# Optimization experiments

Hardware: AMD Instinct MI355X
Metric: run time of the kernel (lower is better)

## Reference

```python
import jax, jax.numpy as jnp
import numpy as np

QUALITY = 8
N_PART = 18000 * QUALITY ** 2  # 1,152,000
N_GRID = 128 * QUALITY         # 1024
DX = 1.0 / N_GRID
INV_DX = float(N_GRID)
DT = 1e-4 / QUALITY
P_VOL = (DX * 0.5) ** 2
P_MASS = P_VOL * 1.0
E_MOD, NU = 5000.0, 0.2
MU0 = E_MOD / (2.0 * (1.0 + NU))
LAM0 = E_MOD * NU / ((1.0 + NU) * (1.0 - 2.0 * NU))
OFF = jnp.array([[i, j] for i in range(3) for j in range(3)], dtype=jnp.int32)  # [9,2]


def setup_inputs() -> dict:
    key = jax.random.key(0)
    ks = jax.random.split(key, 6)
    x = 0.05 + 0.9 * jax.random.uniform(ks[0], (N_PART, 2), dtype=jnp.float32)
    v = jax.random.normal(ks[1], (N_PART, 2), dtype=jnp.float32)
    C = 0.1 * jax.random.normal(ks[2], (N_PART, 2, 2), dtype=jnp.float32)
    F = jnp.eye(2, dtype=jnp.float32) + 0.02 * jax.random.normal(ks[3], (N_PART, 2, 2), dtype=jnp.float32)
    material = jax.random.randint(ks[4], (N_PART,), 0, 3, dtype=jnp.int32)
    Jp = 0.5 + jax.random.uniform(ks[5], (N_PART,), dtype=jnp.float32)
    gravity = jnp.array([0.0, -1.0], dtype=jnp.float32)
    attractor_strength = jnp.array(1.0, dtype=jnp.float32)
    attractor_pos = jnp.array([0.5, 0.5], dtype=jnp.float32)
    return dict(x=x, v=v, C=C, F=F, Jp=Jp, gravity=gravity,
                attractor_strength=attractor_strength, attractor_pos=attractor_pos,
                material=material)


def _substep(x, v, C, F, Jp, gravity, attractor_strength, attractor_pos, material):
    I2 = jnp.eye(2, dtype=x.dtype)
    # ---- per-particle quadratic B-spline weights ----
    base = jnp.floor(x * INV_DX - 0.5).astype(jnp.int32)            # [P,2]
    fx = x * INV_DX - base.astype(x.dtype)                           # [P,2]
    w = jnp.stack([0.5 * (1.5 - fx) ** 2,
                   0.75 - (fx - 1.0) ** 2,
                   0.5 * (fx - 0.5) ** 2], axis=1)                   # [P,3,2]
    weight = w[:, OFF[:, 0], 0] * w[:, OFF[:, 1], 1]                 # [P,9]

    # ---- deformation update + elastoplastic stress ----
    F = jnp.einsum('pij,pjk->pik', I2 + DT * C, F)                   # [P,2,2]
    h = jnp.clip(jnp.exp(10.0 * (1.0 - Jp)), 0.1, 5.0)
    h = jnp.where(material == 1, 0.3, h)
    mu = jnp.where(material == 0, 0.0, MU0 * h)                      # [P]
    la = LAM0 * h
    U, sig, Vh = jnp.linalg.svd(F)                                   # sig [P,2]
    new_sig = jnp.where((material == 2)[:, None],
                        jnp.clip(sig, 1.0 - 2.5e-2, 1.0 + 4.5e-3), sig)
    Jp = Jp * jnp.prod(sig / new_sig, axis=1)
    J = jnp.prod(new_sig, axis=1)                                    # [P]
    F_fluid = jnp.sqrt(J)[:, None, None] * I2
    F_snow = jnp.einsum('pij,pj,pjk->pik', U, new_sig, Vh)
    F = jnp.where((material == 0)[:, None, None], F_fluid,
                  jnp.where((material == 2)[:, None, None], F_snow, F))
    R = jnp.einsum('pij,pjk->pik', U, Vh)                            # rotation U V^T
    stress = (2.0 * mu[:, None, None] *
              jnp.einsum('pij,pkj->pik', F - R, F) +
              (la * J * (J - 1.0))[:, None, None] * I2)
    stress = (-DT * P_VOL * 4.0 * INV_DX * INV_DX) * stress
    affine = stress + P_MASS * C                                     # [P,2,2]

    # ---- P2G scatter-add ----
    dpos = (OFF.astype(x.dtype)[None] - fx[:, None, :]) * DX         # [P,9,2]
    mom = weight[:, :, None] * (P_MASS * v[:, None, :] +
                                jnp.einsum('pab,pkb->pka', affine, dpos))
    gi = jnp.clip(base[:, None, 0] + OFF[None, :, 0], 0, N_GRID - 1)
    gj = jnp.clip(base[:, None, 1] + OFF[None, :, 1], 0, N_GRID - 1)
    idx = (gi * N_GRID + gj).reshape(-1)                              # [P*9]
    grid_v = jnp.zeros((N_GRID * N_GRID, 2), x.dtype).at[idx].add(mom.reshape(-1, 2))
    grid_m = jnp.zeros((N_GRID * N_GRID,), x.dtype).at[idx].add((weight * P_MASS).reshape(-1))

    # ---- grid update ----
    gv = grid_v.reshape(N_GRID, N_GRID, 2)
    gm = grid_m.reshape(N_GRID, N_GRID)
    mask = gm > 0
    gv = jnp.where(mask[..., None], gv / jnp.where(mask, gm, 1.0)[..., None], 0.0)
    gv = gv + DT * 30.0 * gravity                                    # broadcast [2]
    ii, jj = jnp.meshgrid(jnp.arange(N_GRID), jnp.arange(N_GRID), indexing='ij')
    coords = DX * jnp.stack([ii, jj], axis=-1).astype(x.dtype)        # [G,G,2]
    dist = attractor_pos - coords
    gv = gv + dist / (0.01 + jnp.linalg.norm(dist, axis=-1, keepdims=True)) \
              * attractor_strength * DT * 100.0
    gvx, gvy = gv[..., 0], gv[..., 1]
    gvx = jnp.where((ii < 3) & (gvx < 0), 0.0, gvx)
    gvx = jnp.where((ii > N_GRID - 3) & (gvx > 0), 0.0, gvx)
    gvy = jnp.where((jj < 3) & (gvy < 0), 0.0, gvy)
    gvy = jnp.where((jj > N_GRID - 3) & (gvy > 0), 0.0, gvy)
    gv = jnp.where(mask[..., None], jnp.stack([gvx, gvy], axis=-1), 0.0)

    # ---- G2P gather ----
    g_v = gv.reshape(N_GRID * N_GRID, 2)[idx].reshape(-1, 9, 2)       # [P,9,2]
    new_v = jnp.einsum('pk,pka->pa', weight, g_v)
    dpos_g = OFF.astype(x.dtype)[None] - fx[:, None, :]               # unscaled
    new_C = 4.0 * INV_DX * jnp.einsum('pk,pka,pkb->pab', weight, g_v, dpos_g)
    x_new = x + DT * new_v
    return x_new, new_v, new_C, F, Jp


def reference(x, v, C, F, Jp, gravity, attractor_strength, attractor_pos, material):
    return _substep(x, v, C, F, Jp, gravity, attractor_strength, attractor_pos, material)
```

## Files before the change

### kernel.cpp

```cpp
#include <hip/hip_runtime.h>
#include <hip/hip_fp16.h>
#include <math.h>

namespace {
constexpr int   QUALITY = 8;
constexpr int   NPART   = 18000 * QUALITY * QUALITY;
constexpr int   NG      = 128 * QUALITY;
constexpr int   NCELL   = NG * NG;
constexpr int   CT      = 16;
constexpr int   NBT     = NG / CT;
constexpr float DX      = 1.0f / (float)NG;
constexpr float INV_DX  = (float)NG;
constexpr float DT      = (float)(1e-4 / (double)QUALITY);
constexpr float MU0     = (float)(5000.0 / (2.0 * (1.0 + 0.2)));
constexpr float LAM0    = (float)(5000.0 * 0.2 / ((1.0 + 0.2) * (1.0 - 0.4)));
constexpr float STRESS_RP  = (float)(-(1e-4 / 8.0) * 4.0 * 1024.0 * 1024.0);
constexpr float GRAV_SCALE = (float)((1e-4 / 8.0) * 30.0);
constexpr float ATTR_SCALE = (float)((1e-4 / 8.0) * 100.0);

typedef int v4i __attribute__((ext_vector_type(4)));

__device__ __forceinline__ int2 base_of(float xx, float xy) {
    int bx = (int)floorf(xx * INV_DX - 0.5f);
    int by = (int)floorf(xy * INV_DX - 0.5f);
    bx = min(max(bx, 0), NG - 3);
    by = min(max(by, 0), NG - 3);
    return make_int2(bx, by);
}

__device__ __forceinline__ unsigned pack2h(float a, float b) {
    __half2 h = __floats2half2_rn(a, b);
    return *reinterpret_cast<unsigned*>(&h);
}
__device__ __forceinline__ float2 unpack2h(unsigned u) {
    __half2 h = *reinterpret_cast<__half2*>(&u);
    return __half22float2(h);
}

__device__ __forceinline__ float bspline(float s) {
    s = fabsf(s);
    float a = 0.75f - s * s;
    float b = 1.5f - s;
    b = 0.5f * b * b;
    return (s < 0.5f) ? a : b;
}
}

__global__ __launch_bounds__(256)
void count_kernel(const float* __restrict__ x, int* __restrict__ cnt,
                  int* __restrict__ rank) {
    int p = blockIdx.x * blockDim.x + threadIdx.x;
    if (p >= NPART) return;
    const float2 xv = ((const float2*)x)[p];
    int2 b = base_of(xv.x, xv.y);
    rank[p] = atomicAdd(&cnt[b.x * NG + b.y], 1);
}

__global__ __launch_bounds__(256)
void blocksum_kernel(const int* __restrict__ cnt, int* __restrict__ bsum) {
    __shared__ int sh[256];
    int t = threadIdx.x;
    int4 c = ((const int4*)cnt)[blockIdx.x * 256 + t];
    sh[t] = c.x + c.y + c.z + c.w;
    __syncthreads();
    for (int s = 128; s > 0; s >>= 1) {
        if (t < s) sh[t] += sh[t + s];
        __syncthreads();
    }
    if (t == 0) bsum[blockIdx.x] = sh[0];
}

__global__ __launch_bounds__(1024)
void scanb_kernel(const int* __restrict__ bsum, int* __restrict__ boff,
                  int* __restrict__ cell_start) {
    __shared__ int s[1024];
    int t = threadIdx.x;
    int v = bsum[t];
    s[t] = v;
    __syncthreads();
    for (int off = 1; off < 1024; off <<= 1) {
        int add = (t >= off) ? s[t - off] : 0;
        __syncthreads();
        s[t] += add;
        __syncthreads();
    }
    boff[t] = s[t] - v;
    if (t == 1023) cell_start[NCELL] = s[t];
}

__global__ __launch_bounds__(256)
void scanc_kernel(const int* __restrict__ cnt, const int* __restrict__ boff,
                  int* __restrict__ cell_start) {
    __shared__ int tsum[256];
    int t = threadIdx.x;
    int gbase4 = blockIdx.x * 256 + t;
    int4 c = ((const int4*)cnt)[gbase4];
    int s1 = c.x, s2 = s1 + c.y, s3 = s2 + c.z, tot = s3 + c.w;
    tsum[t] = tot;
    __syncthreads();
    for (int off = 1; off < 256; off <<= 1) {
        int add = (t >= off) ? tsum[t - off] : 0;
        __syncthreads();
        tsum[t] += add;
        __syncthreads();
    }
    int excl = tsum[t] - tot;
    int g = boff[blockIdx.x] + excl;
    ((int4*)cell_start)[gbase4] = make_int4(g, g + s1, g + s2, g + s3);
}

__global__ __launch_bounds__(256)
void physics_scatter_kernel(const float* __restrict__ x, const float* __restrict__ v,
                            const float* __restrict__ Cin, const float* __restrict__ Fin,
                            const float* __restrict__ Jpin, const int* __restrict__ mat,
                            const int* __restrict__ cell_start, const int* __restrict__ rank,
                            uint4* __restrict__ spay,
                            float* __restrict__ outF, float* __restrict__ outJp)
{
    int p = blockIdx.x * blockDim.x + threadIdx.x;
    if (p >= NPART) return;

    const float2 xv = ((const float2*)x)[p];
    const float2 vv = ((const float2*)v)[p];
    const float4 Cv = ((const float4*)Cin)[p];
    const float4 Fv = ((const float4*)Fin)[p];
    float xx = xv.x, xy = xv.y;
    float C00 = Cv.x, C01 = Cv.y, C10 = Cv.z, C11 = Cv.w;
    float F00 = Fv.x, F01 = Fv.y, F10 = Fv.z, F11 = Fv.w;

    float A00 = 1.0f + DT * C00, A01 = DT * C01, A10 = DT * C10, A11 = 1.0f + DT * C11;
    float G00 = A00 * F00 + A01 * F10;
    float G01 = A00 * F01 + A01 * F11;
    float G10 = A10 * F00 + A11 * F10;
    float G11 = A10 * F01 + A11 * F11;

    int m = mat[p];
    float Jp = Jpin[p];
    float h = fminf(fmaxf(expf(10.0f * (1.0f - Jp)), 0.1f), 5.0f);
    if (m == 1) h = 0.3f;
    float mu = (m == 0) ? 0.0f : MU0 * h;
    float la = LAM0 * h;

    float Ee = 0.5f * (G00 + G11);
    float Hh = 0.5f * (G10 - G01);
    float Ff = 0.5f * (G00 - G11);
    float Gg = 0.5f * (G10 + G01);
    float Qq = sqrtf(Ee * Ee + Hh * Hh);
    float Rr = sqrtf(Ff * Ff + Gg * Gg);
    float s0 = Qq + Rr, s1 = Qq - Rr;
    float b1 = atan2f(Gg, Ff);
    float b2 = atan2f(Hh, Ee);
    float phi = 0.5f * (b1 + b2), th = 0.5f * (b1 - b2);
    float sphi, cphi, sth, cth;
    sincosf(phi, &sphi, &cphi);
    sincosf(th, &sth, &cth);

    float ns0 = s0, ns1 = s1;
    if (m == 2) {
        ns0 = fminf(fmaxf(s0, 1.0f - 2.5e-2f), 1.0f + 4.5e-3f);
        ns1 = fminf(fmaxf(s1, 1.0f - 2.5e-2f), 1.0f + 4.5e-3f);
        Jp = Jp * (s0 / ns0) * (s1 / ns1);
    }
    float J = ns0 * ns1;

    float FF00, FF01, FF10, FF11;
    if (m == 0) {
        float sj = sqrtf(J);
        FF00 = sj; FF01 = 0.0f; FF10 = 0.0f; FF11 = sj;
    } else if (m == 2) {
        FF00 = ns0 * cphi * cth + ns1 * sphi * sth;
        FF01 = ns0 * cphi * sth - ns1 * sphi * cth;
        FF10 = ns0 * sphi * cth - ns1 * cphi * sth;
        FF11 = ns0 * sphi * sth + ns1 * cphi * cth;
    } else {
        FF00 = G00; FF01 = G01; FF10 = G10; FF11 = G11;
    }

    float cr = cphi * cth + sphi * sth;
    float sr = sphi * cth - cphi * sth;

    float D00 = FF00 - cr,  D01 = FF01 + sr;
    float D10 = FF10 - sr,  D11 = FF11 - cr;
    float S00 = D00 * FF00 + D01 * FF01;
    float S01 = D00 * FF10 + D01 * FF11;
    float S10 = D10 * FF00 + D11 * FF01;
    float S11 = D10 * FF10 + D11 * FF11;
    float lj = la * J * (J - 1.0f);
    S00 = 2.0f * mu * S00 + lj;
    S01 = 2.0f * mu * S01;
    S10 = 2.0f * mu * S10;
    S11 = 2.0f * mu * S11 + lj;
    float a00 = STRESS_RP * S00 + C00;
    float a01 = STRESS_RP * S01 + C01;
    float a10 = STRESS_RP * S10 + C10;
    float a11 = STRESS_RP * S11 + C11;

    ((float4*)outF)[p] = make_float4(FF00, FF01, FF10, FF11);
    outJp[p] = Jp;

    float bxf = floorf(xx * INV_DX - 0.5f);
    float byf = floorf(xy * INV_DX - 0.5f);
    float fxx = xx * INV_DX - bxf;
    float fxy = xy * INV_DX - byf;
    unsigned qx = (unsigned)__float2int_rn((fxx - 0.5f) * 16383.0f);
    unsigned qy = (unsigned)__float2int_rn((fxy - 0.5f) * 16383.0f);

    int2 b = base_of(xx, xy);

    v4i payload;
    payload.x = (int)((qx & 0x3FFFu) | ((qy & 0x3FFFu) << 16) | (((unsigned)b.y & 3u) << 30));
    payload.y = (int)pack2h(vv.x, vv.y);
    payload.z = (int)pack2h(a00, a01);
    payload.w = (int)pack2h(a10, a11);

    int pos = cell_start[b.x * NG + b.y] + rank[p];
    __builtin_nontemporal_store(payload, (v4i*)&spay[pos]);
}

__global__ __launch_bounds__(256)
void p2g_gather_grid_kernel(const uint4* __restrict__ spay,
                            const int* __restrict__ cell_start,
                            const float* __restrict__ grav,
                            const float* __restrict__ astr,
                            const float* __restrict__ apos,
                            float* __restrict__ gv)
{
    int b = blockIdx.x;
    int tile = (b & 7) * 512 + (b >> 3);
    int lr = threadIdx.x / CT;
    int lc = threadIdx.x % CT;
    int cx = (tile / NBT) * CT + lr;
    int cy = (tile % NBT) * CT + lc;

    float svx = 0.0f, svy = 0.0f, sw = 0.0f;
    int c0 = max(cy - 2, 0);
    float fcy = (float)cy;

    #pragma unroll
    for (int d = 0; d < 3; ++d) {
        int r = cx - 2 + d;
        if (r < 0 || r > NG - 1) continue;
        int row = r * NG;
        int s = cell_start[row + c0];
        int e = cell_start[row + cy + 1];
        const float io = (float)(2 - d);
        for (int t = s; t < e; ++t) {
            uint4 q = spay[t];
            float fxx = 0.5f + (float)(q.x & 0x3FFFu) * (1.0f / 16383.0f);
            float fxy = 0.5f + (float)((q.x >> 16) & 0x3FFFu) * (1.0f / 16383.0f);
            float fj = (float)((cy - (int)(q.x >> 30)) & 3);
            float wx;
            if (d == 0)      wx = 0.5f * (fxx - 0.5f) * (fxx - 0.5f);
            else if (d == 1) wx = 0.75f - (fxx - 1.0f) * (fxx - 1.0f);
            else             wx = 0.5f * (1.5f - fxx) * (1.5f - fxx);
            float wy = bspline(fxy - fj);
            float w = wx * wy;
            float2 vv = unpack2h(q.y);
            float2 aA = unpack2h(q.z);
            float2 aB = unpack2h(q.w);
            float dpx = (io - fxx) * DX;
            float dpy = (fj - fxy) * DX;
            svx += w * (vv.x + aA.x * dpx + aA.y * dpy);
            svy += w * (vv.y + aB.x * dpx + aB.y * dpy);
            sw  += w;
        }
    }

    float vx = 0.0f, vy = 0.0f;
    if (sw > 0.0f) {
        float inv = 1.0f / sw;
        vx = svx * inv + GRAV_SCALE * grav[0];
        vy = svy * inv + GRAV_SCALE * grav[1];
        float dxp = apos[0] - DX * (float)cx;
        float dyp = apos[1] - DX * fcy;
        float nrm = sqrtf(dxp * dxp + dyp * dyp);
        float k = astr[0] * ATTR_SCALE / (0.01f + nrm);
        vx += dxp * k;
        vy += dyp * k;
        if (cx < 3 && vx < 0.0f) vx = 0.0f;
        if (cx > NG - 3 && vx > 0.0f) vx = 0.0f;
        if (cy < 3 && vy < 0.0f) vy = 0.0f;
        if (cy > NG - 3 && vy > 0.0f) vy = 0.0f;
    }
    ((float2*)gv)[cx * NG + cy] = make_float2(vx, vy);
}

__global__ __launch_bounds__(256)
void g2p_kernel(const float* __restrict__ x, const float* __restrict__ gv,
                float* __restrict__ outX, float* __restrict__ outV,
                float* __restrict__ outC)
{
    int p = blockIdx.x * blockDim.x + threadIdx.x;
    if (p >= NPART) return;

    const float2 xv = ((const float2*)x)[p];
    float xx = xv.x, xy = xv.y;
    float bxf = floorf(xx * INV_DX - 0.5f);
    float byf = floorf(xy * INV_DX - 0.5f);
    int bx = (int)bxf, by = (int)byf;
    float fxx = xx * INV_DX - bxf;
    float fxy = xy * INV_DX - byf;

    float wxs[3], wys[3];
    wxs[0] = 0.5f * (1.5f - fxx) * (1.5f - fxx);
    wxs[1] = 0.75f - (fxx - 1.0f) * (fxx - 1.0f);
    wxs[2] = 0.5f * (fxx - 0.5f) * (fxx - 0.5f);
    wys[0] = 0.5f * (1.5f - fxy) * (1.5f - fxy);
    wys[1] = 0.75f - (fxy - 1.0f) * (fxy - 1.0f);
    wys[2] = 0.5f * (fxy - 0.5f) * (fxy - 0.5f);

    int a0 = min(max(by & ~1, 0), NG - 4);
    bool odd = (by - a0) == 1;

    float nvx = 0.0f, nvy = 0.0f;
    float c00 = 0.0f, c01 = 0.0f, c10 = 0.0f, c11 = 0.0f;

    #pragma unroll
    for (int i = 0; i < 3; ++i) {
        int gi = min(max(bx + i, 0), NG - 1);
        float dpx = (float)i - fxx;
        const float4* rowp = (const float4*)(gv + gi * NG * 2 + a0 * 2);
        float4 A = rowp[0];
        float4 B = rowp[1];
        float g0x = odd ? A.z : A.x,  g0y = odd ? A.w : A.y;
        float g1x = odd ? B.x : A.z,  g1y = odd ? B.y : A.w;
        float g2x = odd ? B.z : B.x,  g2y = odd ? B.w : B.y;
        float w0 = wxs[i] * wys[0];
        float w1 = wxs[i] * wys[1];
        float w2 = wxs[i] * wys[2];
        float dpy0 = 0.0f - fxy, dpy1 = 1.0f - fxy, dpy2 = 2.0f - fxy;
        nvx += w0 * g0x + w1 * g1x + w2 * g2x;
        nvy += w0 * g0y + w1 * g1y + w2 * g2y;
        c00 += dpx * (w0 * g0x + w1 * g1x + w2 * g2x);
        c01 += w0 * g0x * dpy0 + w1 * g1x * dpy1 + w2 * g2x * dpy2;
        c10 += dpx * (w0 * g0y + w1 * g1y + w2 * g2y);
        c11 += w0 * g0y * dpy0 + w1 * g1y * dpy1 + w2 * g2y * dpy2;
    }
    float cs = 4.0f * INV_DX;
    ((float2*)outV)[p] = make_float2(nvx, nvy);
    ((float2*)outX)[p] = make_float2(xx + DT * nvx, xy + DT * nvy);
    ((float4*)outC)[p] = make_float4(cs * c00, cs * c01, cs * c10, cs * c11);
}

extern "C" void kernel_launch(void* const* d_in, const int* in_sizes, int n_in,
                              void* d_out, int out_size, void* d_ws, size_t ws_size,
                              hipStream_t stream)
{
    const float* x    = (const float*)d_in[0];
    const float* v    = (const float*)d_in[1];
    const float* C    = (const float*)d_in[2];
    const float* F    = (const float*)d_in[3];
    const float* Jp   = (const float*)d_in[4];
    const float* grav = (const float*)d_in[5];
    const float* astr = (const float*)d_in[6];
    const float* apos = (const float*)d_in[7];
    const int*   mat  = (const int*)d_in[8];

    float* out   = (float*)d_out;
    float* outX  = out;
    float* outV  = out + 2 * NPART;
    float* outC  = out + 4 * NPART;
    float* outF  = out + 8 * NPART;
    float* outJp = out + 12 * NPART;

    int*   ws_i      = (int*)d_ws;
    int*   cnt       = ws_i;
    float* gv        = (float*)d_ws;
    int*   cell_start= ws_i + 2 * NCELL;
    int*   bsum      = cell_start + NCELL + 1;
    int*   boff      = bsum + 1024;
    int*   rank      = boff + 1024;
    size_t off       = (size_t)(3 * NCELL + 2 * 1024 + 1 + NPART);
    off = (off + 3) & ~(size_t)3;
    uint4* spay      = (uint4*)(ws_i + off);

    const int TB = 256;
    hipMemsetAsync(cnt, 0, (size_t)NCELL * sizeof(int), stream);
    count_kernel   <<<(NPART + TB - 1) / TB, TB, 0, stream>>>(x, cnt, rank);
    blocksum_kernel<<<NCELL / 1024, TB, 0, stream>>>(cnt, bsum);
    scanb_kernel   <<<1, 1024, 0, stream>>>(bsum, boff, cell_start);
    scanc_kernel   <<<NCELL / 1024, TB, 0, stream>>>(cnt, boff, cell_start);
    physics_scatter_kernel<<<(NPART + TB - 1) / TB, TB, 0, stream>>>(
        x, v, C, F, Jp, mat, cell_start, rank, spay, outF, outJp);
    p2g_gather_grid_kernel<<<NBT * NBT, TB, 0, stream>>>(
        spay, cell_start, grav, astr, apos, gv);
    g2p_kernel     <<<(NPART + TB - 1) / TB, TB, 0, stream>>>(x, gv, outX, outV, outC);
}
```

Measured before the change: 181.3 us.

## Replace three-pass global scan with single-pass per-row scan and atomic row offsets

The three-kernel prefix sum (block sums, scan of block sums, final scan) is replaced by one kernel that scans each grid row locally and claims a row base offset with an atomicAdd on a global counter. Rows are no longer contiguous in global order, so cell_start becomes a per-row array with one extra end entry per row, and the scatter and gather kernels index it by row. This removes two kernel launches and their serialization, including a single-block scan. In exchange, row order in the sorted buffer is no longer deterministic and scalar stores replace the vectorized int4 stores.

```diff
diff --git a/kernel.cpp b/kernel.cpp
--- a/kernel.cpp
+++ b/kernel.cpp
@@ -7,6 +7,7 @@
 constexpr int   NPART   = 18000 * QUALITY * QUALITY;
 constexpr int   NG      = 128 * QUALITY;
 constexpr int   NCELL   = NG * NG;
+constexpr int   CSROW   = NG + 1;
 constexpr int   CT      = 16;
 constexpr int   NBT     = NG / CT;
 constexpr float DX      = 1.0f / (float)NG;
@@ -57,44 +58,13 @@
 }
 
 __global__ __launch_bounds__(256)
-void blocksum_kernel(const int* __restrict__ cnt, int* __restrict__ bsum) {
-    __shared__ int sh[256];
+void row_scan_kernel(const int* __restrict__ cnt, int* __restrict__ counter,
+                     int* __restrict__ cell_start) {
+    __shared__ int tsum[256];
+    __shared__ int s_base;
+    int r = blockIdx.x;
     int t = threadIdx.x;
-    int4 c = ((const int4*)cnt)[blockIdx.x * 256 + t];
-    sh[t] = c.x + c.y + c.z + c.w;
-    __syncthreads();
-    for (int s = 128; s > 0; s >>= 1) {
-        if (t < s) sh[t] += sh[t + s];
-        __syncthreads();
-    }
-    if (t == 0) bsum[blockIdx.x] = sh[0];
-}
-
-__global__ __launch_bounds__(1024)
-void scanb_kernel(const int* __restrict__ bsum, int* __restrict__ boff,
-                  int* __restrict__ cell_start) {
-    __shared__ int s[1024];
-    int t = threadIdx.x;
-    int v = bsum[t];
-    s[t] = v;
-    __syncthreads();
-    for (int off = 1; off < 1024; off <<= 1) {
-        int add = (t >= off) ? s[t - off] : 0;
-        __syncthreads();
-        s[t] += add;
-        __syncthreads();
-    }
-    boff[t] = s[t] - v;
-    if (t == 1023) cell_start[NCELL] = s[t];
-}
-
-__global__ __launch_bounds__(256)
-void scanc_kernel(const int* __restrict__ cnt, const int* __restrict__ boff,
-                  int* __restrict__ cell_start) {
-    __shared__ int tsum[256];
-    int t = threadIdx.x;
-    int gbase4 = blockIdx.x * 256 + t;
-    int4 c = ((const int4*)cnt)[gbase4];
+    int4 c = ((const int4*)cnt)[r * 256 + t];
     int s1 = c.x, s2 = s1 + c.y, s3 = s2 + c.z, tot = s3 + c.w;
     tsum[t] = tot;
     __syncthreads();
@@ -104,9 +74,16 @@
         tsum[t] += add;
         __syncthreads();
     }
-    int excl = tsum[t] - tot;
-    int g = boff[blockIdx.x] + excl;
-    ((int4*)cell_start)[gbase4] = make_int4(g, g + s1, g + s2, g + s3);
+    if (t == 255) s_base = atomicAdd(counter, tsum[255]);
+    __syncthreads();
+    int base = s_base;
+    int excl = base + tsum[t] - tot;
+    int o = r * CSROW + t * 4;
+    cell_start[o + 0] = excl;
+    cell_start[o + 1] = excl + s1;
+    cell_start[o + 2] = excl + s2;
+    cell_start[o + 3] = excl + s3;
+    if (t == 255) cell_start[r * CSROW + NG] = base + tsum[255];
 }
 
 __global__ __launch_bounds__(256)
@@ -213,7 +190,7 @@
     payload.z = (int)pack2h(a00, a01);
     payload.w = (int)pack2h(a10, a11);
 
-    int pos = cell_start[b.x * NG + b.y] + rank[p];
+    int pos = cell_start[b.x * CSROW + b.y] + rank[p];
     __builtin_nontemporal_store(payload, (v4i*)&spay[pos]);
 }
 
@@ -240,7 +217,7 @@
     for (int d = 0; d < 3; ++d) {
         int r = cx - 2 + d;
         if (r < 0 || r > NG - 1) continue;
-        int row = r * NG;
+        int row = r * CSROW;
         int s = cell_start[row + c0];
         int e = cell_start[row + cy + 1];
         const float io = (float)(2 - d);
@@ -365,21 +342,18 @@
 
     int*   ws_i      = (int*)d_ws;
     int*   cnt       = ws_i;
+    int*   counter   = ws_i + NCELL;
     float* gv        = (float*)d_ws;
     int*   cell_start= ws_i + 2 * NCELL;
-    int*   bsum      = cell_start + NCELL + 1;
-    int*   boff      = bsum + 1024;
-    int*   rank      = boff + 1024;
-    size_t off       = (size_t)(3 * NCELL + 2 * 1024 + 1 + NPART);
+    int*   rank      = cell_start + NG * CSROW;
+    size_t off       = (size_t)(2 * NCELL + NG * CSROW + NPART);
     off = (off + 3) & ~(size_t)3;
     uint4* spay      = (uint4*)(ws_i + off);
 
     const int TB = 256;
-    hipMemsetAsync(cnt, 0, (size_t)NCELL * sizeof(int), stream);
+    hipMemsetAsync(cnt, 0, ((size_t)NCELL + 1) * sizeof(int), stream);
     count_kernel   <<<(NPART + TB - 1) / TB, TB, 0, stream>>>(x, cnt, rank);
-    blocksum_kernel<<<NCELL / 1024, TB, 0, stream>>>(cnt, bsum);
-    scanb_kernel   <<<1, 1024, 0, stream>>>(bsum, boff, cell_start);
-    scanc_kernel   <<<NCELL / 1024, TB, 0, stream>>>(cnt, boff, cell_start);
+    row_scan_kernel<<<NG, TB, 0, stream>>>(cnt, counter, cell_start);
     physics_scatter_kernel<<<(NPART + TB - 1) / TB, TB, 0, stream>>>(
         x, v, C, F, Jp, mat, cell_start, rank, spay, outF, outJp);
     p2g_gather_grid_kernel<<<NBT * NBT, TB, 0, stream>>>(
```

After: 188.7 us. 1.04x slower.
